# Kernel tuning notes

Measured on AMD Instinct MI355X. Metric: run time of the kernel, lower is better.

## Reference

```python
import jax, jax.numpy as jnp
import numpy as np

B, NW, D, K = 16384, 32, 64, 512  # batch, n_windows, embedding_dim, codebook_size


def setup_inputs() -> dict:
    key = jax.random.key(0)
    k1, k2 = jax.random.split(key)
    ze = jax.random.normal(k1, (B, NW * D), dtype=jnp.float32)
    codebook = jax.random.normal(k2, (K, D), dtype=jnp.float32)
    return {"ze": ze, "codebook": codebook}


def reference(ze, codebook):
    # window-based VQ: split last dim into NW windows of size D, quantize each
    zew = ze.reshape(B, NW, D)
    # squared distances: ||ze||^2 + ||e||^2 - 2 ze.e^T  -> [B, NW, K]
    sq_norm = (
        jnp.sum(zew * zew, axis=-1, keepdims=True)
        + jnp.sum(codebook * codebook, axis=-1)
        - 2.0 * jnp.einsum("bwd,kd->bwk", zew, codebook)
    )
    indices = jnp.argmin(sq_norm, axis=-1)  # [B, NW]
    zq = codebook[indices].reshape(ze.shape)  # gather + concat over windows

    vq_e_loss = jnp.mean((zq - jax.lax.stop_gradient(ze)) ** 2)
    vq_commit_loss = jnp.mean((jax.lax.stop_gradient(zq) - ze) ** 2)

    # entropy term: counts of each code usage divided by 10 (as in original)
    counts = jnp.bincount(indices.reshape(-1), length=K)
    probs = counts.astype(jnp.float32) / 10.0
    entropy = jnp.sum(probs * jnp.log(probs + 1e-10))
    return indices, zq, vq_e_loss, vq_commit_loss, entropy
```

## Files before the change

kernel.cpp:

```cpp
#include <hip/hip_runtime.h>
#include <math.h>

#define DIM 64
#define KCB 512
#define NWIN 524288
#define ZQN (NWIN * DIM)
#define WPT 256
#define TPB 4
#define NBLK (NWIN / (WPT * TPB))

typedef __attribute__((ext_vector_type(8))) short bf16x8;
typedef __attribute__((ext_vector_type(4))) float f32x4;

__device__ __forceinline__ unsigned bfbits(float f) { return __float_as_uint(f) >> 16; }

__device__ __forceinline__ int4 pack8(float4 a, float4 b) {
    int4 r;
    r.x = (int)(bfbits(a.x) | (__float_as_uint(a.y) & 0xffff0000u));
    r.y = (int)(bfbits(a.z) | (__float_as_uint(a.w) & 0xffff0000u));
    r.z = (int)(bfbits(b.x) | (__float_as_uint(b.y) & 0xffff0000u));
    r.w = (int)(bfbits(b.z) | (__float_as_uint(b.w) & 0xffff0000u));
    return r;
}

__global__ __launch_bounds__(256, 2) void vq_fused_kernel(
    const float* __restrict__ ze, const float* __restrict__ cb,
    float* __restrict__ out_idx, float* __restrict__ zq,
    int* __restrict__ counts, float* __restrict__ lossAcc)
{
    __shared__ int4  bfr[4096];
    __shared__ float norm_s[KCB];
    __shared__ int   idx_s[WPT];
    __shared__ int   hist_s[KCB];
    __shared__ float lpart[4];

    const int t    = threadIdx.x;
    const int lane = t & 63;
    const int wv   = t >> 6;
    const int q    = lane >> 4;
    const int l15  = lane & 15;
    const long blk = blockIdx.x;

    hist_s[t] = 0; hist_s[t + 256] = 0;

    {
        const float4* c4 = (const float4*)cb;
        for (int rr = t; rr < KCB; rr += 256) {
            float s = 0.f;
#pragma unroll
            for (int i = 0; i < 16; ++i) {
                float4 v = c4[rr * 16 + i];
                s += v.x * v.x + v.y * v.y + v.z * v.z + v.w * v.w;
            }
            norm_s[rr] = s;
        }
    }

#pragma unroll
    for (int i = 0; i < 16; ++i) {
        int f = i * 256 + t;
        int L = f & 63, rest = f >> 6, h = rest & 1, c = rest >> 1;
        int n = c * 16 + (L & 15);
        int k = h * 32 + (L >> 4) * 8;
        const float4* s4 = (const float4*)(cb + n * DIM + k);
        bfr[(c * 2 + h) * 64 + L] = pack8(s4[0], s4[1]);
    }
    __syncthreads();

    const float4* z4b = (const float4*)ze;
    float4*       zq4 = (float4*)zq;
    float lsum = 0.f;

    float4 abuf[16];
    {
        const float4* z4 = z4b + blk * TPB * WPT * 16;
#pragma unroll
        for (int tt = 0; tt < 4; ++tt)
#pragma unroll
            for (int h = 0; h < 2; ++h)
#pragma unroll
                for (int i = 0; i < 2; ++i) {
                    int m = wv * 64 + tt * 16 + l15;
                    abuf[tt * 4 + h * 2 + i] = z4[m * 16 + h * 8 + q * 2 + i];
                }
    }

#pragma unroll
    for (int tl = 0; tl < TPB; ++tl) {
        const long g = blk * TPB + tl;

        float4 pre[16];
        if (tl < TPB - 1) {
            const float4* z4 = z4b + (g + 1) * WPT * 16;
#pragma unroll
            for (int tt = 0; tt < 4; ++tt)
#pragma unroll
                for (int h = 0; h < 2; ++h)
#pragma unroll
                    for (int i = 0; i < 2; ++i) {
                        int m = wv * 64 + tt * 16 + l15;
                        pre[tt * 4 + h * 2 + i] = z4[m * 16 + h * 8 + q * 2 + i];
                    }
        }

        bf16x8 afrag[4][2];
        float  znorm[4];
#pragma unroll
        for (int tt = 0; tt < 4; ++tt) {
            float part = 0.f;
#pragma unroll
            for (int h = 0; h < 2; ++h) {
                float4 a0 = abuf[tt * 4 + h * 2], a1 = abuf[tt * 4 + h * 2 + 1];
                part += a0.x*a0.x + a0.y*a0.y + a0.z*a0.z + a0.w*a0.w
                      + a1.x*a1.x + a1.y*a1.y + a1.z*a1.z + a1.w*a1.w;
                afrag[tt][h] = __builtin_bit_cast(bf16x8, pack8(a0, a1));
            }
            part += __shfl_xor(part, 16, 64);
            part += __shfl_xor(part, 32, 64);
            znorm[tt] = part;
        }

        float best[4][4];
#pragma unroll
        for (int tt = 0; tt < 4; ++tt)
#pragma unroll
            for (int r = 0; r < 4; ++r) best[tt][r] = __uint_as_float(0x7e000000u);

        for (int c = 0; c < 32; ++c) {
            bf16x8 b0 = __builtin_bit_cast(bf16x8, bfr[(c * 2 + 0) * 64 + lane]);
            bf16x8 b1 = __builtin_bit_cast(bf16x8, bfr[(c * 2 + 1) * 64 + lane]);
            int   n   = c * 16 + l15;
            float nrm = norm_s[n];
#pragma unroll
            for (int tt = 0; tt < 4; ++tt) {
                f32x4 acc = {0.f, 0.f, 0.f, 0.f};
                acc = __builtin_amdgcn_mfma_f32_16x16x32_bf16(afrag[tt][0], b0, acc, 0, 0, 0);
                acc = __builtin_amdgcn_mfma_f32_16x16x32_bf16(afrag[tt][1], b1, acc, 0, 0, 0);
#pragma unroll
                for (int r = 0; r < 4; ++r) {
                    float sc = fmaf(nrm, 0.5f, -acc[r]);
                    unsigned bb = (__float_as_uint(sc) & ~511u) | (unsigned)n;
                    best[tt][r] = fminf(best[tt][r], __uint_as_float(bb));
                }
            }
        }

#pragma unroll
        for (int tt = 0; tt < 4; ++tt)
#pragma unroll
            for (int r = 0; r < 4; ++r) {
                float v = best[tt][r];
                v = fminf(v, __shfl_xor(v, 1, 64));
                v = fminf(v, __shfl_xor(v, 2, 64));
                v = fminf(v, __shfl_xor(v, 4, 64));
                v = fminf(v, __shfl_xor(v, 8, 64));
                best[tt][r] = v;
            }

        {
            int  r_act = l15 - q * 4;
            bool act   = (r_act >= 0) && (r_act < 4);
#pragma unroll
            for (int tt = 0; tt < 4; ++tt) {
                if (act) {
                    unsigned bb = __float_as_uint(best[tt][r_act]);
                    int   n  = (int)(bb & 511u);
                    float sc = __uint_as_float(bb & ~511u);
                    lsum += fmaf(2.f, sc, znorm[tt]);
                    idx_s[wv * 64 + tt * 16 + l15] = n;
                }
            }
        }
        __syncthreads();

        out_idx[g * WPT + t] = (float)idx_s[t];
        atomicAdd(&hist_s[idx_s[t]], 1);

        {
            const long zb = g * WPT * 16;
#pragma unroll
            for (int it = 0; it < 16; ++it) {
                int w_loc = it * 16 + (t >> 4);
                int j  = t & 15;
                int n  = idx_s[w_loc];
                int c  = n >> 4, ln = n & 15;
                int h  = j >> 3;
                int q2 = (j >> 1) & 3;
                int4 v = bfr[(c * 2 + h) * 64 + q2 * 16 + ln];
                int a  = (j & 1) ? v.z : v.x;
                int b  = (j & 1) ? v.w : v.y;
                float4 o;
                o.x = __uint_as_float((unsigned)a << 16);
                o.y = __uint_as_float((unsigned)a & 0xffff0000u);
                o.z = __uint_as_float((unsigned)b << 16);
                o.w = __uint_as_float((unsigned)b & 0xffff0000u);
                zq4[zb + (long)w_loc * 16 + j] = o;
            }
        }
        __syncthreads();

        if (tl < TPB - 1) {
#pragma unroll
            for (int i = 0; i < 16; ++i) abuf[i] = pre[i];
        }
    }

#pragma unroll
    for (int off = 32; off; off >>= 1) lsum += __shfl_down(lsum, off, 64);
    if (lane == 0) lpart[wv] = lsum;
    __syncthreads();
    if (t == 0) atomicAdd(lossAcc, lpart[0] + lpart[1] + lpart[2] + lpart[3]);

    int h0 = hist_s[t], h1 = hist_s[t + 256];
    if (h0) atomicAdd(&counts[t], h0);
    if (h1) atomicAdd(&counts[t + 256], h1);
}

__global__ __launch_bounds__(512) void vq_finalize_kernel(
    const int* __restrict__ counts, const float* __restrict__ lossAcc,
    float* __restrict__ outs)
{
    __shared__ float partial[8];
    const int t = threadIdx.x;

    float p = (float)counts[t] * 0.1f;
    float term = p * logf(p + 1e-10f);
#pragma unroll
    for (int off = 32; off; off >>= 1) term += __shfl_down(term, off, 64);
    if ((t & 63) == 0) partial[t >> 6] = term;
    __syncthreads();
    if (t == 0) {
        float e = 0.f;
#pragma unroll
        for (int i = 0; i < 8; ++i) e += partial[i];
        float loss = lossAcc[0] / (float)ZQN;
        outs[0] = loss;
        outs[1] = loss;
        outs[2] = e;
    }
}

extern "C" void kernel_launch(void* const* d_in, const int* in_sizes, int n_in,
                              void* d_out, int out_size, void* d_ws, size_t ws_size,
                              hipStream_t stream) {
    const float* ze = (const float*)d_in[0];
    const float* cb = (const float*)d_in[1];
    float* out = (float*)d_out;

    float* out_idx = out;
    float* out_zq  = out + NWIN;
    float* out_scl = out + NWIN + (long)ZQN;

    int*   counts  = (int*)d_ws;
    float* lossAcc = (float*)((char*)d_ws + KCB * sizeof(int));
    hipMemsetAsync(d_ws, 0, KCB * sizeof(int) + sizeof(float), stream);

    vq_fused_kernel<<<NBLK, 256, 0, stream>>>(ze, cb, out_idx, out_zq, counts, lossAcc);
    vq_finalize_kernel<<<1, KCB, 0, stream>>>(counts, lossAcc, out_scl);
}
```

Baseline: 285.2 us.

## Fold codebook norm into MFMA accumulator, negate A, use 512-thread blocks

The half codebook norm now seeds the MFMA accumulator, and the A fragment's bf16 sign bits are flipped, so the MFMA output is the score directly and the per-element fma is gone. Blocks grow to 512 threads (8 waves) handling 512 windows per tile with 2 tiles per block. The ze prefetch for the next tile is moved after the argmin, which removes the separate 16-register prefetch buffer. Two codebook chunks are processed per iteration to expose more independent MFMAs, at the cost of more live accumulator registers and less overlap of global loads with compute.

```diff
diff --git a/kernel.cpp b/kernel.cpp
--- a/kernel.cpp
+++ b/kernel.cpp
@@ -5,8 +5,8 @@
 #define KCB 512
 #define NWIN 524288
 #define ZQN (NWIN * DIM)
-#define WPT 256
-#define TPB 4
+#define WPT 512
+#define TPB 2
 #define NBLK (NWIN / (WPT * TPB))
 
 typedef __attribute__((ext_vector_type(8))) short bf16x8;
@@ -23,7 +23,7 @@
     return r;
 }
 
-__global__ __launch_bounds__(256, 2) void vq_fused_kernel(
+__global__ __launch_bounds__(512, 4) void vq_fused_kernel(
     const float* __restrict__ ze, const float* __restrict__ cb,
     float* __restrict__ out_idx, float* __restrict__ zq,
     int* __restrict__ counts, float* __restrict__ lossAcc)
@@ -32,7 +32,7 @@
     __shared__ float norm_s[KCB];
     __shared__ int   idx_s[WPT];
     __shared__ int   hist_s[KCB];
-    __shared__ float lpart[4];
+    __shared__ float lpart[8];
 
     const int t    = threadIdx.x;
     const int lane = t & 63;
@@ -41,31 +41,28 @@
     const int l15  = lane & 15;
     const long blk = blockIdx.x;
 
-    hist_s[t] = 0; hist_s[t + 256] = 0;
+    hist_s[t] = 0;
 
     {
         const float4* c4 = (const float4*)cb;
-        for (int rr = t; rr < KCB; rr += 256) {
-            float s = 0.f;
-#pragma unroll
-            for (int i = 0; i < 16; ++i) {
-                float4 v = c4[rr * 16 + i];
-                s += v.x * v.x + v.y * v.y + v.z * v.z + v.w * v.w;
-            }
-            norm_s[rr] = s;
-        }
-    }
-
-#pragma unroll
-    for (int i = 0; i < 16; ++i) {
-        int f = i * 256 + t;
+        float s = 0.f;
+#pragma unroll
+        for (int i = 0; i < 16; ++i) {
+            float4 v = c4[t * 16 + i];
+            s += v.x * v.x + v.y * v.y + v.z * v.z + v.w * v.w;
+        }
+        norm_s[t] = 0.5f * s;
+    }
+
+#pragma unroll
+    for (int i = 0; i < 8; ++i) {
+        int f = i * 512 + t;
         int L = f & 63, rest = f >> 6, h = rest & 1, c = rest >> 1;
         int n = c * 16 + (L & 15);
         int k = h * 32 + (L >> 4) * 8;
         const float4* s4 = (const float4*)(cb + n * DIM + k);
         bfr[(c * 2 + h) * 64 + L] = pack8(s4[0], s4[1]);
     }
-    __syncthreads();
 
     const float4* z4b = (const float4*)ze;
     float4*       zq4 = (float4*)zq;
@@ -74,34 +71,20 @@
     float4 abuf[16];
     {
         const float4* z4 = z4b + blk * TPB * WPT * 16;
+        const int m = wv * 64 + l15;
 #pragma unroll
         for (int tt = 0; tt < 4; ++tt)
 #pragma unroll
             for (int h = 0; h < 2; ++h)
 #pragma unroll
-                for (int i = 0; i < 2; ++i) {
-                    int m = wv * 64 + tt * 16 + l15;
-                    abuf[tt * 4 + h * 2 + i] = z4[m * 16 + h * 8 + q * 2 + i];
-                }
-    }
+                for (int i = 0; i < 2; ++i)
+                    abuf[tt * 4 + h * 2 + i] = z4[(m + tt * 16) * 16 + h * 8 + q * 2 + i];
+    }
+    __syncthreads();
 
 #pragma unroll
     for (int tl = 0; tl < TPB; ++tl) {
         const long g = blk * TPB + tl;
-
-        float4 pre[16];
-        if (tl < TPB - 1) {
-            const float4* z4 = z4b + (g + 1) * WPT * 16;
-#pragma unroll
-            for (int tt = 0; tt < 4; ++tt)
-#pragma unroll
-                for (int h = 0; h < 2; ++h)
-#pragma unroll
-                    for (int i = 0; i < 2; ++i) {
-                        int m = wv * 64 + tt * 16 + l15;
-                        pre[tt * 4 + h * 2 + i] = z4[m * 16 + h * 8 + q * 2 + i];
-                    }
-        }
 
         bf16x8 afrag[4][2];
         float  znorm[4];
@@ -113,7 +96,10 @@
                 float4 a0 = abuf[tt * 4 + h * 2], a1 = abuf[tt * 4 + h * 2 + 1];
                 part += a0.x*a0.x + a0.y*a0.y + a0.z*a0.z + a0.w*a0.w
                       + a1.x*a1.x + a1.y*a1.y + a1.z*a1.z + a1.w*a1.w;
-                afrag[tt][h] = __builtin_bit_cast(bf16x8, pack8(a0, a1));
+                int4 p = pack8(a0, a1);
+                p.x ^= 0x80008000; p.y ^= 0x80008000;
+                p.z ^= 0x80008000; p.w ^= 0x80008000;
+                afrag[tt][h] = __builtin_bit_cast(bf16x8, p);
             }
             part += __shfl_xor(part, 16, 64);
             part += __shfl_xor(part, 32, 64);
@@ -126,23 +112,42 @@
 #pragma unroll
             for (int r = 0; r < 4; ++r) best[tt][r] = __uint_as_float(0x7e000000u);
 
-        for (int c = 0; c < 32; ++c) {
-            bf16x8 b0 = __builtin_bit_cast(bf16x8, bfr[(c * 2 + 0) * 64 + lane]);
-            bf16x8 b1 = __builtin_bit_cast(bf16x8, bfr[(c * 2 + 1) * 64 + lane]);
-            int   n   = c * 16 + l15;
-            float nrm = norm_s[n];
-#pragma unroll
-            for (int tt = 0; tt < 4; ++tt) {
-                f32x4 acc = {0.f, 0.f, 0.f, 0.f};
-                acc = __builtin_amdgcn_mfma_f32_16x16x32_bf16(afrag[tt][0], b0, acc, 0, 0, 0);
-                acc = __builtin_amdgcn_mfma_f32_16x16x32_bf16(afrag[tt][1], b1, acc, 0, 0, 0);
+        for (int cp = 0; cp < 16; ++cp) {
+            f32x4 e0[4], e1[4];
+            {
+                const int c = 2 * cp;
+                bf16x8 b0 = __builtin_bit_cast(bf16x8, bfr[(c * 2 + 0) * 64 + lane]);
+                bf16x8 b1 = __builtin_bit_cast(bf16x8, bfr[(c * 2 + 1) * 64 + lane]);
+                float nh = norm_s[c * 16 + l15];
+                f32x4 nrm4 = {nh, nh, nh, nh};
+#pragma unroll
+                for (int tt = 0; tt < 4; ++tt) {
+                    e0[tt] = __builtin_amdgcn_mfma_f32_16x16x32_bf16(afrag[tt][0], b0, nrm4, 0, 0, 0);
+                    e0[tt] = __builtin_amdgcn_mfma_f32_16x16x32_bf16(afrag[tt][1], b1, e0[tt], 0, 0, 0);
+                }
+            }
+            {
+                const int c = 2 * cp + 1;
+                bf16x8 b0 = __builtin_bit_cast(bf16x8, bfr[(c * 2 + 0) * 64 + lane]);
+                bf16x8 b1 = __builtin_bit_cast(bf16x8, bfr[(c * 2 + 1) * 64 + lane]);
+                float nh = norm_s[c * 16 + l15];
+                f32x4 nrm4 = {nh, nh, nh, nh};
+#pragma unroll
+                for (int tt = 0; tt < 4; ++tt) {
+                    e1[tt] = __builtin_amdgcn_mfma_f32_16x16x32_bf16(afrag[tt][0], b0, nrm4, 0, 0, 0);
+                    e1[tt] = __builtin_amdgcn_mfma_f32_16x16x32_bf16(afrag[tt][1], b1, e1[tt], 0, 0, 0);
+                }
+            }
+            const unsigned n0 = (unsigned)(2 * cp) * 16 + (unsigned)l15;
+            const unsigned n1 = n0 + 16;
+#pragma unroll
+            for (int tt = 0; tt < 4; ++tt)
 #pragma unroll
                 for (int r = 0; r < 4; ++r) {
-                    float sc = fmaf(nrm, 0.5f, -acc[r]);
-                    unsigned bb = (__float_as_uint(sc) & ~511u) | (unsigned)n;
-                    best[tt][r] = fminf(best[tt][r], __uint_as_float(bb));
-                }
-            }
+                    float p0 = __uint_as_float((__float_as_uint(e0[tt][r]) & ~511u) | n0);
+                    float p1 = __uint_as_float((__float_as_uint(e1[tt][r]) & ~511u) | n1);
+                    best[tt][r] = fminf(fminf(best[tt][r], p0), p1);
+                }
         }
 
 #pragma unroll
@@ -171,6 +176,18 @@
                 }
             }
         }
+
+        if (tl < TPB - 1) {
+            const float4* z4 = z4b + (g + 1) * WPT * 16;
+            const int m = wv * 64 + l15;
+#pragma unroll
+            for (int tt = 0; tt < 4; ++tt)
+#pragma unroll
+                for (int h = 0; h < 2; ++h)
+#pragma unroll
+                    for (int i = 0; i < 2; ++i)
+                        abuf[tt * 4 + h * 2 + i] = z4[(m + tt * 16) * 16 + h * 8 + q * 2 + i];
+        }
         __syncthreads();
 
         out_idx[g * WPT + t] = (float)idx_s[t];
@@ -180,7 +197,7 @@
             const long zb = g * WPT * 16;
 #pragma unroll
             for (int it = 0; it < 16; ++it) {
-                int w_loc = it * 16 + (t >> 4);
+                int w_loc = it * 32 + (t >> 4);
                 int j  = t & 15;
                 int n  = idx_s[w_loc];
                 int c  = n >> 4, ln = n & 15;
@@ -198,22 +215,20 @@
             }
         }
         __syncthreads();
-
-        if (tl < TPB - 1) {
-#pragma unroll
-            for (int i = 0; i < 16; ++i) abuf[i] = pre[i];
-        }
     }
 
 #pragma unroll
     for (int off = 32; off; off >>= 1) lsum += __shfl_down(lsum, off, 64);
     if (lane == 0) lpart[wv] = lsum;
     __syncthreads();
-    if (t == 0) atomicAdd(lossAcc, lpart[0] + lpart[1] + lpart[2] + lpart[3]);
-
-    int h0 = hist_s[t], h1 = hist_s[t + 256];
+    if (t == 0) {
+        float s = 0.f;
+#pragma unroll
+        for (int i = 0; i < 8; ++i) s += lpart[i];
+        atomicAdd(lossAcc, s);
+    }
+    int h0 = hist_s[t];
     if (h0) atomicAdd(&counts[t], h0);
-    if (h1) atomicAdd(&counts[t + 256], h1);
 }
 
 __global__ __launch_bounds__(512) void vq_finalize_kernel(
@@ -255,6 +270,6 @@
     float* lossAcc = (float*)((char*)d_ws + KCB * sizeof(int));
     hipMemsetAsync(d_ws, 0, KCB * sizeof(int) + sizeof(float), stream);
 
-    vq_fused_kernel<<<NBLK, 256, 0, stream>>>(ze, cb, out_idx, out_zq, counts, lossAcc);
+    vq_fused_kernel<<<NBLK, 512, 0, stream>>>(ze, cb, out_idx, out_zq, counts, lossAcc);
     vq_finalize_kernel<<<1, KCB, 0, stream>>>(counts, lossAcc, out_scl);
 }
```

After: 278.3 us. 1.02x faster.
